# Performance work log

Hardware: AMD Instinct MI355X
Metric: run time of the kernel (lower is better)

## Reference

```python
import jax, jax.numpy as jnp
import numpy as np

B, D, C, H = 16384, 512, 4096, 1024

def setup_inputs() -> dict:
    key = jax.random.key(0)
    k1, k2, k3, k4 = jax.random.split(key, 4)
    x = jax.random.normal(k1, (B, D), dtype=jnp.float32)
    centers = jax.random.normal(k2, (C, D), dtype=jnp.float32)
    # nn.Linear(C, H): weight [H, C], bias [H]
    W1 = jax.random.normal(k3, (H, C), dtype=jnp.float32) * (1.0 / np.sqrt(C))
    b1 = jax.random.normal(k4, (H,), dtype=jnp.float32) * 0.01
    return {"x": x, "centers": centers, "W1": W1, "b1": b1, "sigma": 1}


def reference(x, centers, W1, b1, sigma):
    sigma = jnp.float32(sigma)
    # Pairwise Euclidean distances via dot-product expansion (fused, no [B,C,D] tensor)
    x2 = jnp.sum(x * x, axis=-1, keepdims=True)            # [B, 1]
    c2 = jnp.sum(centers * centers, axis=-1)               # [C]
    xc = x @ centers.T                                     # [B, C]
    d2 = jnp.maximum(x2 + c2[None, :] - 2.0 * xc, 0.0)
    dists = jnp.sqrt(d2)                                   # [B, C]
    # Note: original uses exp(-dists / (2*sigma)) with UNSQUARED distance
    phi = jnp.exp(-dists / (2.0 * sigma))
    out = jax.nn.sigmoid(phi @ W1.T + b1)                  # [B, H]
    return out
```

## Files before the change

kernel.cpp:

```cpp
#include <hip/hip_runtime.h>
#include <hip/hip_bf16.h>

#define B_ROWS 16384
#define D_DIM  512
#define C_DIM  4096
#define H_DIM  1024

typedef __attribute__((ext_vector_type(8))) short  bf16x8;
typedef __attribute__((ext_vector_type(8))) unsigned short u16x8;
typedef __attribute__((ext_vector_type(4))) float  f32x4;

#define GLB __attribute__((address_space(1)))
#define LDS __attribute__((address_space(3)))

#define MFMA(d, va, vb) d = __builtin_amdgcn_mfma_f32_16x16x32_bf16(va, vb, d, 0, 0, 0)
#define LGKM0() asm volatile("s_waitcnt lgkmcnt(0)" ::: "memory")

__device__ __forceinline__ unsigned short f2bf(float f) {
    unsigned int u = __float_as_uint(f);
    unsigned int r = (u + 0x7FFFu + ((u >> 16) & 1u)) >> 16;
    return (unsigned short)r;
}

__device__ __forceinline__ void async16(const void* g, void* l) {
    __builtin_amdgcn_global_load_lds((const GLB unsigned int*)g,
                                     (LDS unsigned int*)l, 16, 0, 0);
}

__device__ __forceinline__ float read_sigma(const int* p) {
    int v = *p;
    if (v >= 1 && v < (1 << 20)) return (float)v;
    return __int_as_float(v);
}

__global__ __launch_bounds__(256) void prep_rows(const float* __restrict__ in,
                                                 unsigned short* __restrict__ outb,
                                                 float* __restrict__ out2) {
    int row  = blockIdx.x * 4 + (threadIdx.x >> 6);
    int lane = threadIdx.x & 63;
    const float4* p = (const float4*)(in + (size_t)row * D_DIM) + lane * 2;
    float4 a = p[0], b = p[1];
    float s = a.x*a.x + a.y*a.y + a.z*a.z + a.w*a.w
            + b.x*b.x + b.y*b.y + b.z*b.z + b.w*b.w;
    u16x8 o = { f2bf(a.x), f2bf(a.y), f2bf(a.z), f2bf(a.w),
                f2bf(b.x), f2bf(b.y), f2bf(b.z), f2bf(b.w) };
    *(u16x8*)(outb + (size_t)row * D_DIM + lane * 8) = o;
#pragma unroll
    for (int off = 32; off; off >>= 1) s += __shfl_down(s, off, 64);
    if (lane == 0) out2[row] = s;
}

__global__ __launch_bounds__(256) void conv_bf16(const float* __restrict__ in,
                                                 unsigned short* __restrict__ outb,
                                                 int n8) {
    int i = blockIdx.x * 256 + threadIdx.x;
    if (i >= n8) return;
    const float4* p = (const float4*)in + (size_t)i * 2;
    float4 a = p[0], b = p[1];
    u16x8 o = { f2bf(a.x), f2bf(a.y), f2bf(a.z), f2bf(a.w),
                f2bf(b.x), f2bf(b.y), f2bf(b.z), f2bf(b.w) };
    *((u16x8*)outb + i) = o;
}

__device__ __forceinline__ void stage_half(const unsigned short* __restrict__ g,
                                           int ld, int rowBase, int k0,
                                           unsigned short* lds, int tid) {
#pragma unroll
    for (int i = 0; i < 2; i++) {
        int idx = i * 512 + tid;
        int row = idx >> 3;
        int cc  = (idx & 7) ^ (row & 7);
        const unsigned short* src = g + (size_t)(rowBase + row) * ld + k0 + cc * 8;
        unsigned short* dst = lds + (i * 512 + (tid & 448)) * 8;
        async16(src, dst);
    }
}

__device__ __forceinline__ bf16x8 frag(const unsigned short* T, int r, int kc) {
    return *(const bf16x8*)(T + r * 64 + ((kc ^ (r & 7)) << 3));
}

__device__ __forceinline__ void ktile(unsigned short* __restrict__ Ap,
                                      unsigned short* __restrict__ Bp,
                                      const unsigned short* __restrict__ gA, int lda, int aRow0,
                                      const unsigned short* __restrict__ gB, int ldb, int bRow0,
                                      int kNext, bool doStage,
                                      f32x4 (&acc)[8][4], int tid, int l, int AR, int BC) {
    const int lr = l & 15, hi = l >> 4;
    bf16x8 a[4][2], b0[2][2], b1[2][2];

#pragma unroll
    for (int m = 0; m < 4; m++) { int r = AR + m * 16 + lr;
#pragma unroll
        for (int kk = 0; kk < 2; kk++) a[m][kk] = frag(Ap, r, kk * 4 + hi); }
#pragma unroll
    for (int n = 0; n < 2; n++) { int r = BC + n * 16 + lr;
#pragma unroll
        for (int kk = 0; kk < 2; kk++) b0[n][kk] = frag(Bp, r, kk * 4 + hi); }
    __builtin_amdgcn_s_barrier();
    LGKM0();
    __builtin_amdgcn_s_setprio(1);
#pragma unroll
    for (int kk = 0; kk < 2; kk++)
#pragma unroll
        for (int m = 0; m < 4; m++)
#pragma unroll
            for (int n = 0; n < 2; n++) MFMA(acc[m][n], a[m][kk], b0[n][kk]);
    __builtin_amdgcn_s_setprio(0);
    __builtin_amdgcn_s_barrier();

#pragma unroll
    for (int n = 0; n < 2; n++) { int r = BC + (n + 2) * 16 + lr;
#pragma unroll
        for (int kk = 0; kk < 2; kk++) b1[n][kk] = frag(Bp, r, kk * 4 + hi); }
    __builtin_amdgcn_s_barrier();
    LGKM0();
    __builtin_amdgcn_s_setprio(1);
#pragma unroll
    for (int kk = 0; kk < 2; kk++)
#pragma unroll
        for (int m = 0; m < 4; m++)
#pragma unroll
            for (int n = 0; n < 2; n++) MFMA(acc[m][2 + n], a[m][kk], b1[n][kk]);
    __builtin_amdgcn_s_setprio(0);
    __builtin_amdgcn_s_barrier();

#pragma unroll
    for (int m = 0; m < 4; m++) { int r = AR + (m + 4) * 16 + lr;
#pragma unroll
        for (int kk = 0; kk < 2; kk++) a[m][kk] = frag(Ap, r, kk * 4 + hi); }
    if (doStage) {
        stage_half(gB, ldb, bRow0,       kNext, Bp,        tid);
        stage_half(gB, ldb, bRow0 + 128, kNext, Bp + 8192, tid);
    }
    __builtin_amdgcn_s_barrier();
    LGKM0();
    __builtin_amdgcn_s_setprio(1);
#pragma unroll
    for (int kk = 0; kk < 2; kk++)
#pragma unroll
        for (int m = 0; m < 4; m++)
#pragma unroll
            for (int n = 0; n < 2; n++) MFMA(acc[4 + m][n], a[m][kk], b0[n][kk]);
    __builtin_amdgcn_s_setprio(0);
    __builtin_amdgcn_s_barrier();

    if (doStage) {
        stage_half(gA, lda, aRow0,       kNext, Ap,        tid);
        stage_half(gA, lda, aRow0 + 128, kNext, Ap + 8192, tid);
    }
    __builtin_amdgcn_s_barrier();
    __builtin_amdgcn_s_setprio(1);
#pragma unroll
    for (int kk = 0; kk < 2; kk++)
#pragma unroll
        for (int m = 0; m < 4; m++)
#pragma unroll
            for (int n = 0; n < 2; n++) MFMA(acc[4 + m][2 + n], a[m][kk], b1[n][kk]);
    __builtin_amdgcn_s_setprio(0);
    asm volatile("s_waitcnt vmcnt(8)" ::: "memory");
    __builtin_amdgcn_s_barrier();
}

__device__ __forceinline__ void gemm_core(const unsigned short* __restrict__ gA, int lda, int aRow0,
                                          const unsigned short* __restrict__ gB, int ldb, int bRow0,
                                          int nt, f32x4 (&acc)[8][4],
                                          unsigned short (&As)[2][16384],
                                          unsigned short (&Bs)[2][16384],
                                          int tid, int l, int AR, int BC) {
    stage_half(gA, lda, aRow0,       0,  As[0],        tid);
    stage_half(gA, lda, aRow0 + 128, 0,  As[0] + 8192, tid);
    stage_half(gB, ldb, bRow0,       0,  Bs[0],        tid);
    stage_half(gB, ldb, bRow0 + 128, 0,  Bs[0] + 8192, tid);
    stage_half(gA, lda, aRow0,       64, As[1],        tid);
    stage_half(gA, lda, aRow0 + 128, 64, As[1] + 8192, tid);
    stage_half(gB, ldb, bRow0,       64, Bs[1],        tid);
    stage_half(gB, ldb, bRow0 + 128, 64, Bs[1] + 8192, tid);
    asm volatile("s_waitcnt vmcnt(8)" ::: "memory");
    __builtin_amdgcn_s_barrier();

    for (int t = 0; t < nt; t += 2) {
        ktile(As[0], Bs[0], gA, lda, aRow0, gB, ldb, bRow0, (t + 2) * 64, t + 2 < nt,
              acc, tid, l, AR, BC);
        ktile(As[1], Bs[1], gA, lda, aRow0, gB, ldb, bRow0, (t + 3) * 64, t + 3 < nt,
              acc, tid, l, AR, BC);
    }
}

__global__ __launch_bounds__(512) void gemm1_kernel(const unsigned short* __restrict__ xb,
                                                    const unsigned short* __restrict__ cb,
                                                    const float* __restrict__ x2,
                                                    const float* __restrict__ c2,
                                                    const int* __restrict__ sigp,
                                                    unsigned short* __restrict__ phi) {
    __shared__ unsigned short As[2][16384];
    __shared__ unsigned short Bs[2][16384];
    int tid = threadIdx.x;
    int nwg = gridDim.x, cpx = nwg >> 3, bid = blockIdx.x;
    int nb = (bid & 7) * cpx + (bid >> 3);
    const int nbx = C_DIM / 256;
    int aRow0 = (nb / nbx) * 256, bRow0 = (nb % nbx) * 256;
    int l = tid & 63, wid = tid >> 6;
    int AR = (wid >> 2) * 128, BC = (wid & 3) * 64;

    f32x4 acc[8][4] = {};
    gemm_core(xb, D_DIM, aRow0, cb, D_DIM, bRow0, D_DIM / 64, acc, As, Bs, tid, l, AR, BC);

    float inv2s = 0.5f / read_sigma(sigp);
    int lr = l & 15, hi = l >> 4;
#pragma unroll
    for (int m = 0; m < 8; m++) {
#pragma unroll
        for (int j = 0; j < 4; j++) {
            int row = aRow0 + AR + m * 16 + hi * 4 + j;
            float xr = x2[row];
#pragma unroll
            for (int n = 0; n < 4; n++) {
                int col = bRow0 + BC + n * 16 + lr;
                float d2 = fmaxf(xr + c2[col] - 2.0f * acc[m][n][j], 0.0f);
                float ph = __expf(-__builtin_sqrtf(d2) * inv2s);
                phi[(size_t)row * C_DIM + col] = f2bf(ph);
            }
        }
    }
}

__global__ __launch_bounds__(512) void gemm2_kernel(const unsigned short* __restrict__ phi,
                                                    const unsigned short* __restrict__ wb,
                                                    const float* __restrict__ b1,
                                                    float* __restrict__ out) {
    __shared__ unsigned short As[2][16384];
    __shared__ unsigned short Bs[2][16384];
    int tid = threadIdx.x;
    int nwg = gridDim.x, cpx = nwg >> 3, bid = blockIdx.x;
    int nb = (bid & 7) * cpx + (bid >> 3);
    const int nbx = H_DIM / 256;
    int aRow0 = (nb / nbx) * 256, bRow0 = (nb % nbx) * 256;
    int l = tid & 63, wid = tid >> 6;
    int AR = (wid >> 2) * 128, BC = (wid & 3) * 64;

    f32x4 acc[8][4] = {};
    gemm_core(phi, C_DIM, aRow0, wb, C_DIM, bRow0, C_DIM / 64, acc, As, Bs, tid, l, AR, BC);

    int lr = l & 15, hi = l >> 4;
#pragma unroll
    for (int m = 0; m < 8; m++) {
#pragma unroll
        for (int j = 0; j < 4; j++) {
            int row = aRow0 + AR + m * 16 + hi * 4 + j;
#pragma unroll
            for (int n = 0; n < 4; n++) {
                int col = bRow0 + BC + n * 16 + lr;
                float z = acc[m][n][j] + b1[col];
                out[(size_t)row * H_DIM + col] = 1.0f / (1.0f + __expf(-z));
            }
        }
    }
}

extern "C" void kernel_launch(void* const* d_in, const int* in_sizes, int n_in,
                              void* d_out, int out_size, void* d_ws, size_t ws_size,
                              hipStream_t stream) {
    const float* x       = (const float*)d_in[0];
    const float* centers = (const float*)d_in[1];
    const float* W1      = (const float*)d_in[2];
    const float* b1      = (const float*)d_in[3];
    const int*   sig     = (const int*)d_in[4];
    float* out = (float*)d_out;

    char* ws = (char*)d_ws;
    unsigned short* phi = (unsigned short*)(ws);
    unsigned short* xb  = (unsigned short*)(ws + 134217728);
    unsigned short* cb  = (unsigned short*)(ws + 150994944);
    unsigned short* wb  = (unsigned short*)(ws + 155189248);
    float* x2 = (float*)(ws + 163577856);
    float* c2 = (float*)(ws + 163643392);

    prep_rows<<<B_ROWS / 4, 256, 0, stream>>>(x, xb, x2);
    prep_rows<<<C_DIM / 4, 256, 0, stream>>>(centers, cb, c2);
    conv_bf16<<<(H_DIM * C_DIM / 8 + 255) / 256, 256, 0, stream>>>(W1, wb, H_DIM * C_DIM / 8);

    gemm1_kernel<<<(B_ROWS / 256) * (C_DIM / 256), 512, 0, stream>>>(xb, cb, x2, c2, sig, phi);
    gemm2_kernel<<<(B_ROWS / 256) * (H_DIM / 256), 512, 0, stream>>>(phi, wb, b1, out);
}
```

Before: 337.2 us.

## Restagger A/B prefetch so A loads one tile ahead and B two

Restructures the GEMM k-loop pipeline. A is now prefetched only one tile ahead into the other A buffer, spread across the first two MFMA phases. B is still prefetched two tiles ahead into the buffer just consumed, spread across the last two phases. Vmcnt waits are adjusted to match. The aim is to spread global-to-LDS traffic more evenly across the MFMA phases and shorten the prologue, at the risk of exposing A-load latency and adding hazards from reading and writing shared buffers in the same tile.

```diff
diff --git a/kernel.cpp b/kernel.cpp
--- a/kernel.cpp
+++ b/kernel.cpp
@@ -14,6 +14,7 @@
 #define LDS __attribute__((address_space(3)))
 
 #define MFMA(d, va, vb) d = __builtin_amdgcn_mfma_f32_16x16x32_bf16(va, vb, d, 0, 0, 0)
+#define BAR()   __builtin_amdgcn_s_barrier()
 #define LGKM0() asm volatile("s_waitcnt lgkmcnt(0)" ::: "memory")
 
 __device__ __forceinline__ unsigned short f2bf(float f) {
@@ -80,11 +81,13 @@
     return *(const bf16x8*)(T + r * 64 + ((kc ^ (r & 7)) << 3));
 }
 
-__device__ __forceinline__ void ktile(unsigned short* __restrict__ Ap,
-                                      unsigned short* __restrict__ Bp,
+__device__ __forceinline__ void ktile(const unsigned short* __restrict__ Ard,
+                                      const unsigned short* __restrict__ Brd,
+                                      unsigned short* __restrict__ Awr,
+                                      unsigned short* __restrict__ Bwr,
                                       const unsigned short* __restrict__ gA, int lda, int aRow0,
                                       const unsigned short* __restrict__ gB, int ldb, int bRow0,
-                                      int kNext, bool doStage,
+                                      int kA, int kB, bool stageA, bool stageB,
                                       f32x4 (&acc)[8][4], int tid, int l, int AR, int BC) {
     const int lr = l & 15, hi = l >> 4;
     bf16x8 a[4][2], b0[2][2], b1[2][2];
@@ -92,13 +95,14 @@
 #pragma unroll
     for (int m = 0; m < 4; m++) { int r = AR + m * 16 + lr;
 #pragma unroll
-        for (int kk = 0; kk < 2; kk++) a[m][kk] = frag(Ap, r, kk * 4 + hi); }
+        for (int kk = 0; kk < 2; kk++) a[m][kk] = frag(Ard, r, kk * 4 + hi); }
 #pragma unroll
     for (int n = 0; n < 2; n++) { int r = BC + n * 16 + lr;
 #pragma unroll
-        for (int kk = 0; kk < 2; kk++) b0[n][kk] = frag(Bp, r, kk * 4 + hi); }
-    __builtin_amdgcn_s_barrier();
-    LGKM0();
+        for (int kk = 0; kk < 2; kk++) b0[n][kk] = frag(Brd, r, kk * 4 + hi); }
+    if (stageA) stage_half(gA, lda, aRow0, kA, Awr, tid);
+    asm volatile("s_waitcnt lgkmcnt(8)" ::: "memory");
+    BAR(); LGKM0();
     __builtin_amdgcn_s_setprio(1);
 #pragma unroll
     for (int kk = 0; kk < 2; kk++)
@@ -107,14 +111,14 @@
 #pragma unroll
             for (int n = 0; n < 2; n++) MFMA(acc[m][n], a[m][kk], b0[n][kk]);
     __builtin_amdgcn_s_setprio(0);
-    __builtin_amdgcn_s_barrier();
+    BAR();
 
 #pragma unroll
     for (int n = 0; n < 2; n++) { int r = BC + (n + 2) * 16 + lr;
 #pragma unroll
-        for (int kk = 0; kk < 2; kk++) b1[n][kk] = frag(Bp, r, kk * 4 + hi); }
-    __builtin_amdgcn_s_barrier();
-    LGKM0();
+        for (int kk = 0; kk < 2; kk++) b1[n][kk] = frag(Brd, r, kk * 4 + hi); }
+    if (stageA) stage_half(gA, lda, aRow0 + 128, kA, Awr + 8192, tid);
+    BAR(); LGKM0();
     __builtin_amdgcn_s_setprio(1);
 #pragma unroll
     for (int kk = 0; kk < 2; kk++)
@@ -123,18 +127,14 @@
 #pragma unroll
             for (int n = 0; n < 2; n++) MFMA(acc[m][2 + n], a[m][kk], b1[n][kk]);
     __builtin_amdgcn_s_setprio(0);
-    __builtin_amdgcn_s_barrier();
+    BAR();
 
 #pragma unroll
     for (int m = 0; m < 4; m++) { int r = AR + (m + 4) * 16 + lr;
 #pragma unroll
-        for (int kk = 0; kk < 2; kk++) a[m][kk] = frag(Ap, r, kk * 4 + hi); }
-    if (doStage) {
-        stage_half(gB, ldb, bRow0,       kNext, Bp,        tid);
-        stage_half(gB, ldb, bRow0 + 128, kNext, Bp + 8192, tid);
-    }
-    __builtin_amdgcn_s_barrier();
-    LGKM0();
+        for (int kk = 0; kk < 2; kk++) a[m][kk] = frag(Ard, r, kk * 4 + hi); }
+    if (stageB) stage_half(gB, ldb, bRow0, kB, Bwr, tid);
+    BAR(); LGKM0();
     __builtin_amdgcn_s_setprio(1);
 #pragma unroll
     for (int kk = 0; kk < 2; kk++)
@@ -143,13 +143,15 @@
 #pragma unroll
             for (int n = 0; n < 2; n++) MFMA(acc[4 + m][n], a[m][kk], b0[n][kk]);
     __builtin_amdgcn_s_setprio(0);
-    __builtin_amdgcn_s_barrier();
-
-    if (doStage) {
-        stage_half(gA, lda, aRow0,       kNext, Ap,        tid);
-        stage_half(gA, lda, aRow0 + 128, kNext, Ap + 8192, tid);
-    }
-    __builtin_amdgcn_s_barrier();
+    BAR();
+
+    if (stageB) {
+        stage_half(gB, ldb, bRow0 + 128, kB, Bwr + 8192, tid);
+        asm volatile("s_waitcnt vmcnt(4)" ::: "memory");
+    } else {
+        asm volatile("s_waitcnt vmcnt(0)" ::: "memory");
+    }
+    BAR();
     __builtin_amdgcn_s_setprio(1);
 #pragma unroll
     for (int kk = 0; kk < 2; kk++)
@@ -158,8 +160,7 @@
 #pragma unroll
             for (int n = 0; n < 2; n++) MFMA(acc[4 + m][2 + n], a[m][kk], b1[n][kk]);
     __builtin_amdgcn_s_setprio(0);
-    asm volatile("s_waitcnt vmcnt(8)" ::: "memory");
-    __builtin_amdgcn_s_barrier();
+    BAR();
 }
 
 __device__ __forceinline__ void gemm_core(const unsigned short* __restrict__ gA, int lda, int aRow0,
@@ -172,17 +173,17 @@
     stage_half(gA, lda, aRow0 + 128, 0,  As[0] + 8192, tid);
     stage_half(gB, ldb, bRow0,       0,  Bs[0],        tid);
     stage_half(gB, ldb, bRow0 + 128, 0,  Bs[0] + 8192, tid);
-    stage_half(gA, lda, aRow0,       64, As[1],        tid);
-    stage_half(gA, lda, aRow0 + 128, 64, As[1] + 8192, tid);
     stage_half(gB, ldb, bRow0,       64, Bs[1],        tid);
     stage_half(gB, ldb, bRow0 + 128, 64, Bs[1] + 8192, tid);
-    asm volatile("s_waitcnt vmcnt(8)" ::: "memory");
+    asm volatile("s_waitcnt vmcnt(4)" ::: "memory");
     __builtin_amdgcn_s_barrier();
 
-    for (int t = 0; t < nt; t += 2) {
-        ktile(As[0], Bs[0], gA, lda, aRow0, gB, ldb, bRow0, (t + 2) * 64, t + 2 < nt,
+    for (int u = 0; u < nt; u += 2) {
+        ktile(As[0], Bs[0], As[1], Bs[0], gA, lda, aRow0, gB, ldb, bRow0,
+              (u + 1) * 64, (u + 2) * 64, u + 1 < nt, u + 2 < nt,
               acc, tid, l, AR, BC);
-        ktile(As[1], Bs[1], gA, lda, aRow0, gB, ldb, bRow0, (t + 3) * 64, t + 3 < nt,
+        ktile(As[1], Bs[1], As[0], Bs[1], gA, lda, aRow0, gB, ldb, bRow0,
+              (u + 2) * 64, (u + 3) * 64, u + 2 < nt, u + 3 < nt,
               acc, tid, l, AR, BC);
     }
 }
```

Measured after the change: 344.6 us. 2.2% more time.
